# Optimization experiments

Hardware: AMD Instinct MI355X
Metric: run time of the kernel (lower is better)

Reference implementation:

```python
import jax, jax.numpy as jnp
import numpy as np

TEXT_VOCAB = 32000
CB = 1024          # audio_codebook_size
NCB = 8            # audio_num_codebooks
H = 2048           # hidden_size
NH = 16            # attention heads
NKV = 4            # kv heads (GQA)
HD = H // NH       # head dim = 128
FF = 8192          # ffn intermediate
L = 2              # num layers
EPS = 1e-5


def rmsnorm(x, w):
    v = jnp.mean(x * x, axis=-1, keepdims=True)
    return x * jax.lax.rsqrt(v + EPS) * w


def rope(x, pos):
    # x: [B,S,h,d], rotate-half style RoPE
    d = x.shape[-1]
    inv = 1.0 / (10000.0 ** (jnp.arange(0, d, 2, dtype=jnp.float32) / d))
    ang = pos[:, None] * inv[None, :]                 # [S, d/2]
    cos = jnp.cos(ang)[None, :, None, :]
    sin = jnp.sin(ang)[None, :, None, :]
    x1, x2 = x[..., : d // 2], x[..., d // 2 :]
    return jnp.concatenate([x1 * cos - x2 * sin, x2 * cos + x1 * sin], axis=-1)


def attention(x, wq, wk, wv, wo, pos, mask_bias):
    B, S, _ = x.shape
    q = (x @ wq).reshape(B, S, NH, HD)
    k = (x @ wk).reshape(B, S, NKV, HD)
    v = (x @ wv).reshape(B, S, NKV, HD)
    q = rope(q, pos)
    k = rope(k, pos)
    k = jnp.repeat(k, NH // NKV, axis=2)
    v = jnp.repeat(v, NH // NKV, axis=2)
    scores = jnp.einsum('bqhd,bkhd->bhqk', q, k) / np.float32(np.sqrt(HD))
    p = jax.nn.softmax(scores + mask_bias, axis=-1)
    o = jnp.einsum('bhqk,bkhd->bqhd', p, v).reshape(B, S, NH * HD)
    return o @ wo


def mlp(x, wfc, wproj):
    return jax.nn.silu(x @ wfc) @ wproj


def setup_inputs() -> dict:
    key = jax.random.key(0)
    ks = jax.random.split(key, 20)
    s = 0.02
    inp = {
        'input_ids': jax.random.randint(ks[0], (1, 2048), 0, TEXT_VOCAB + CB, dtype=jnp.int64 if jax.config.jax_enable_x64 else jnp.int32),
        'vocab_emb': jax.random.normal(ks[1], (TEXT_VOCAB, H), jnp.float32) * s,
        'audio_emb': jax.random.normal(ks[2], (NCB * CB, H), jnp.float32) * s,
        'ln_in_text': jnp.ones((L, H), jnp.float32),
        'ln_in_audio': jnp.ones((L, H), jnp.float32),
        'ln_post_text': jnp.ones((L, H), jnp.float32),
        'ln_post_audio': jnp.ones((L, H), jnp.float32),
        'wq': jax.random.normal(ks[3], (L, H, NH * HD), jnp.float32) * s,
        'wk': jax.random.normal(ks[4], (L, H, NKV * HD), jnp.float32) * s,
        'wv': jax.random.normal(ks[5], (L, H, NKV * HD), jnp.float32) * s,
        'wo': jax.random.normal(ks[6], (L, NH * HD, H), jnp.float32) * s,
        'wfc_text': jax.random.normal(ks[7], (L, H, FF), jnp.float32) * s,
        'wproj_text': jax.random.normal(ks[8], (L, FF, H), jnp.float32) * s,
        'wfc_audio': jax.random.normal(ks[9], (L, H, FF), jnp.float32) * s,
        'wproj_audio': jax.random.normal(ks[10], (L, FF, H), jnp.float32) * s,
        'ln_f': jnp.ones((H,), jnp.float32),
    }
    return inp


def reference(input_ids, vocab_emb, audio_emb, ln_in_text, ln_in_audio,
              ln_post_text, ln_post_audio, wq, wk, wv, wo,
              wfc_text, wproj_text, wfc_audio, wproj_audio, ln_f):
    B, S = input_ids.shape
    amask = input_ids > TEXT_VOCAB - 1                      # [B,S] audio-token mask
    text_tok = jnp.where(amask, TEXT_VOCAB - 1, input_ids)
    text_e = vocab_emb[text_tok]                            # [B,S,H]
    audio_tok = jnp.where(amask, input_ids - TEXT_VOCAB, 0)
    shift = (jnp.arange(NCB) * CB)[:, None, None]           # [NCB,1,1]
    audio_e = audio_emb[audio_tok[None] + shift].sum(0)     # sum over codebooks -> [B,S,H]
    h = jnp.where(amask[..., None], audio_e, text_e)

    pos = jnp.arange(S, dtype=jnp.float32)
    causal = jnp.tril(jnp.ones((S, S), bool))
    mask_bias = jnp.where(causal, 0.0, -1e9).astype(jnp.float32)[None, None]
    m = amask[..., None]

    for i in range(L):
        res = h
        hn = jnp.where(m, rmsnorm(h, ln_in_audio[i]), rmsnorm(h, ln_in_text[i]))
        h = res + attention(hn, wq[i], wk[i], wv[i], wo[i], pos, mask_bias)
        res = h
        t = mlp(rmsnorm(h, ln_post_text[i]), wfc_text[i], wproj_text[i])
        a = mlp(rmsnorm(h, ln_post_audio[i]), wfc_audio[i], wproj_audio[i])
        h = res + jnp.where(m, a, t)

    return rmsnorm(h, ln_f)
```

## Files before the change

kernel.cpp:

```cpp
#include <hip/hip_runtime.h>
#include <hip/hip_bf16.h>
#include <math.h>

#define S_LEN 2048
#define HID   2048

typedef __bf16 bf16x8 __attribute__((ext_vector_type(8)));
typedef float  f32x4  __attribute__((ext_vector_type(4)));

__device__ __forceinline__ unsigned short f2b(float x) {
  __hip_bfloat16 h = __float2bfloat16(x);
  return __builtin_bit_cast(unsigned short, h);
}

__device__ __forceinline__ float block_sum_256(float v) {
  __shared__ float red[4];
  #pragma unroll
  for (int o = 32; o > 0; o >>= 1) v += __shfl_down(v, o, 64);
  if ((threadIdx.x & 63) == 0) red[threadIdx.x >> 6] = v;
  __syncthreads();
  v = red[0] + red[1] + red[2] + red[3];
  __syncthreads();
  return v;
}

__global__ __launch_bounds__(256) void embed_kernel(
    const int* __restrict__ ids, const float* __restrict__ vemb,
    const float* __restrict__ aemb, float* __restrict__ h, int* __restrict__ amask) {
  const int s = blockIdx.x;
  const int id = ids[s];
  const bool am = id > 31999;
  if (threadIdx.x == 0) amask[s] = am ? 1 : 0;
  const int d0 = threadIdx.x * 8;
  float out[8];
  if (am) {
    const int at = id - 32000;
    #pragma unroll
    for (int u = 0; u < 8; u++) out[u] = 0.f;
    for (int cb = 0; cb < 8; cb++) {
      const float* src = aemb + (long)(at + cb * 1024) * HID + d0;
      #pragma unroll
      for (int u = 0; u < 8; u++) out[u] += src[u];
    }
  } else {
    const float* src = vemb + (long)id * HID + d0;
    #pragma unroll
    for (int u = 0; u < 8; u++) out[u] = src[u];
  }
  float* dst = h + (long)s * HID + d0;
  #pragma unroll
  for (int u = 0; u < 8; u++) dst[u] = out[u];
}

__global__ __launch_bounds__(256) void partition_rows(
    const int* __restrict__ ids, int* __restrict__ apos, int* __restrict__ cnt) {
  __shared__ int ca[256];
  __shared__ int sc[257];
  const int t = threadIdx.x;
  int m[8], loc = 0;
  #pragma unroll
  for (int i = 0; i < 8; i++) { m[i] = ids[t * 8 + i] > 31999 ? 1 : 0; loc += m[i]; }
  ca[t] = loc;
  __syncthreads();
  if (t == 0) {
    int run = 0;
    for (int i = 0; i < 256; i++) { sc[i] = run; run += ca[i]; }
    sc[256] = run;
  }
  __syncthreads();
  int off = sc[t];
  #pragma unroll
  for (int i = 0; i < 8; i++) {
    const int s = t * 8 + i;
    if (m[i]) { apos[s] = off; off++; }
    else apos[s] = -1;
  }
  if (t == 0) { cnt[0] = sc[256]; cnt[1] = (sc[256] + 127) & ~127; }
}

__global__ void init_ctrs(int* c) { c[threadIdx.x] = 0; }

__global__ __launch_bounds__(256) void transposew(
    const float* __restrict__ W, int ldw, unsigned short* __restrict__ Wt, int K, int N) {
  __shared__ float t[64][65];
  const int k0 = blockIdx.y * 64, n0 = blockIdx.x * 64;
  const int q = threadIdx.x & 15;
  const int r0 = threadIdx.x >> 4;
  #pragma unroll
  for (int i = 0; i < 4; i++) {
    const int row = r0 + i * 16;
    const float4 v = *(const float4*)(W + (long)(k0 + row) * ldw + n0 + q * 4);
    t[row][q * 4 + 0] = v.x; t[row][q * 4 + 1] = v.y;
    t[row][q * 4 + 2] = v.z; t[row][q * 4 + 3] = v.w;
  }
  __syncthreads();
  #pragma unroll
  for (int i = 0; i < 4; i++) {
    const int n = r0 + i * 16;
    ushort4 o;
    o.x = f2b(t[q * 4 + 0][n]); o.y = f2b(t[q * 4 + 1][n]);
    o.z = f2b(t[q * 4 + 2][n]); o.w = f2b(t[q * 4 + 3][n]);
    *(ushort4*)(Wt + (long)(n0 + n) * K + k0 + q * 4) = o;
  }
}

__global__ __launch_bounds__(256) void rope_table(float* __restrict__ c, float* __restrict__ s_) {
  const int i = blockIdx.x * 256 + threadIdx.x;
  const int pos = i >> 6, j = i & 63;
  const float inv = powf(10000.f, -(float)(2 * j) * (1.f / 128.f));
  const float ang = (float)pos * inv;
  c[i] = cosf(ang);
  s_[i] = sinf(ang);
}

__global__ __launch_bounds__(64) void rope_apply(
    const float* __restrict__ qkv, const float* __restrict__ rc, const float* __restrict__ rs,
    unsigned short* __restrict__ qb, unsigned short* __restrict__ kb) {
  const int s = blockIdx.x;
  const int hh = blockIdx.y;
  const int j = threadIdx.x;
  const float c = rc[s * 64 + j], sn = rs[s * 64 + j];
  const float* base;
  unsigned short* out;
  if (hh < 16) {
    base = qkv + (long)s * 3072 + hh * 128;
    out = qb + (long)s * 2048 + hh * 128;
  } else {
    base = qkv + (long)s * 3072 + 2048 + (hh - 16) * 128;
    out = kb + (long)s * 512 + (hh - 16) * 128;
  }
  const float x1 = base[j], x2 = base[j + 64];
  out[j] = f2b(x1 * c - x2 * sn);
  out[j + 64] = f2b(x2 * c + x1 * sn);
}

__global__ __launch_bounds__(256) void rmsnorm_sel(
    const float* __restrict__ x, const int* __restrict__ amask,
    const float* __restrict__ wt, const float* __restrict__ wa, unsigned short* __restrict__ out) {
  const long s = blockIdx.x;
  const float* xr = x + s * HID;
  const int d0 = threadIdx.x * 8;
  float v[8], ss = 0.f;
  #pragma unroll
  for (int u = 0; u < 8; u++) { v[u] = xr[d0 + u]; ss += v[u] * v[u]; }
  ss = block_sum_256(ss) * (1.f / HID);
  const float rr = rsqrtf(ss + 1e-5f);
  const float* w = amask[s] ? wa : wt;
  #pragma unroll
  for (int u = 0; u < 8; u++) out[s * HID + d0 + u] = f2b(v[u] * rr * w[d0 + u]);
}

__global__ __launch_bounds__(256) void rmsnorm_post(
    const float* __restrict__ x, const int* __restrict__ apos,
    const float* __restrict__ wt, const float* __restrict__ wa,
    unsigned short* __restrict__ hnt, unsigned short* __restrict__ hna_g) {
  const long s = blockIdx.x;
  const float* xr = x + s * HID;
  const int d0 = threadIdx.x * 8;
  float v[8], ss = 0.f;
  #pragma unroll
  for (int u = 0; u < 8; u++) { v[u] = xr[d0 + u]; ss += v[u] * v[u]; }
  ss = block_sum_256(ss) * (1.f / HID);
  const float rr = rsqrtf(ss + 1e-5f);
  const int ap = apos[s];
  #pragma unroll
  for (int u = 0; u < 8; u++) {
    const float xn = v[u] * rr;
    hnt[s * HID + d0 + u] = f2b(xn * wt[d0 + u]);
    if (ap >= 0) hna_g[(long)ap * HID + d0 + u] = f2b(xn * wa[d0 + u]);
  }
}

__global__ __launch_bounds__(256) void rmsnorm_final(
    const float* __restrict__ x, const float* __restrict__ w, float* __restrict__ out) {
  const long s = blockIdx.x;
  const float* xr = x + s * HID;
  const int d0 = threadIdx.x * 8;
  float v[8], ss = 0.f;
  #pragma unroll
  for (int u = 0; u < 8; u++) { v[u] = xr[d0 + u]; ss += v[u] * v[u]; }
  ss = block_sum_256(ss) * (1.f / HID);
  const float rr = rsqrtf(ss + 1e-5f);
  #pragma unroll
  for (int u = 0; u < 8; u++) out[s * HID + d0 + u] = v[u] * rr * w[d0 + u];
}

__device__ __forceinline__ void gload16(const void* g, void* l) {
  __builtin_amdgcn_global_load_lds((const __attribute__((address_space(1))) void*)g,
                                   (__attribute__((address_space(3))) void*)l, 16, 0, 0);
}

#define ABAR() do { __builtin_amdgcn_s_barrier(); \
  asm volatile("" ::: "memory"); __builtin_amdgcn_sched_barrier(0); } while (0)

__global__ __launch_bounds__(256) void attn_pass1(
    const unsigned short* __restrict__ qb, const unsigned short* __restrict__ kb,
    float* __restrict__ mstat, int* __restrict__ ctr, float iscale) {
  __shared__ __align__(16) unsigned short Kb[2][2][128][64];
  __shared__ int s_item;
  const int tid = threadIdx.x;
  const int lane = tid & 63;
  const int w = tid >> 6;
  const int lr = lane & 15;
  const int kg = lane >> 4;
  const int trow = tid >> 3;
  const int tc = tid & 7;

  for (;;) {
    if (tid == 0) s_item = atomicAdd(ctr, 1);
    __syncthreads();
    const int item = s_item;
    __syncthreads();
    if (item >= 512) break;
    const int q64 = 31 - (item >> 4);
    const int h = item & 15;
    const int kvh = h >> 2;
    const int bm = q64 * 64;
    const int nt = (bm >> 7) + 1;

    bf16x8 af_q[4];
    {
      const unsigned short* qr = qb + (long)(bm + w * 16 + lr) * 2048 + h * 128 + kg * 8;
      #pragma unroll
      for (int c = 0; c < 4; c++) af_q[c] = *(const bf16x8*)(qr + c * 32);
    }
    float m[4], l[4];
    #pragma unroll
    for (int r = 0; r < 4; r++) { m[r] = -1e30f; l[r] = 0.f; }

    auto stageK = [&](int buf, int t) {
      const int kv0 = t * 128;
      #pragma unroll
      for (int hh2 = 0; hh2 < 2; hh2++)
        #pragma unroll
        for (int rr = 0; rr < 4; rr++) {
          const int row = trow + rr * 32;
          gload16(kb + (long)(kv0 + row) * 512 + kvh * 128 + hh2 * 64 + ((tc ^ (row & 7)) * 8),
                  &Kb[buf][hh2][row][tc * 8]);
        }
    };

    stageK(0, 0);
    for (int t = 0; t < nt; t++) {
      const bool hn = (t + 1) < nt;
      if (hn) stageK((t + 1) & 1, t + 1);
      if (hn) { asm volatile("s_waitcnt vmcnt(8)" ::: "memory"); }
      else    { asm volatile("s_waitcnt vmcnt(0)" ::: "memory"); }
      ABAR();
      f32x4 acc[8];
      #pragma unroll
      for (int nf = 0; nf < 8; nf++) acc[nf] = (f32x4){0.f, 0.f, 0.f, 0.f};
      #pragma unroll
      for (int c = 0; c < 4; c++) {
        #pragma unroll
        for (int nf = 0; nf < 8; nf++) {
          const int row = nf * 16 + lr;
          bf16x8 bk = *(const bf16x8*)(&Kb[t & 1][c >> 1][row][(((c & 1) * 4 + kg) ^ (row & 7)) * 8]);
          acc[nf] = __builtin_amdgcn_mfma_f32_16x16x32_bf16(af_q[c], bk, acc[nf], 0, 0, 0);
        }
      }
      const bool diag = !hn;
      #pragma unroll
      for (int r = 0; r < 4; r++) {
        const int rowg = bm + w * 16 + kg * 4 + r;
        float sv[8], tmax = -1e30f;
        #pragma unroll
        for (int nf = 0; nf < 8; nf++) {
          float s = acc[nf][r] * iscale;
          const int colg = t * 128 + nf * 16 + lr;
          if (diag && colg > rowg) s = -1e30f;
          sv[nf] = s;
          tmax = fmaxf(tmax, s);
        }
        #pragma unroll
        for (int o = 1; o < 16; o <<= 1) tmax = fmaxf(tmax, __shfl_xor(tmax, o, 64));
        const float mn = fmaxf(m[r], tmax);
        float psum = 0.f;
        #pragma unroll
        for (int nf = 0; nf < 8; nf++) psum += __expf(sv[nf] - mn);
        #pragma unroll
        for (int o = 1; o < 16; o <<= 1) psum += __shfl_xor(psum, o, 64);
        l[r] = l[r] * __expf(m[r] - mn) + psum;
        m[r] = mn;
      }
      ABAR();
    }
    if (lr == 0) {
      #pragma unroll
      for (int r = 0; r < 4; r++)
        mstat[h * 2048 + bm + w * 16 + kg * 4 + r] = m[r] + __logf(l[r]);
    }
    __syncthreads();
  }
}

__global__ __launch_bounds__(512, 1) void attn_pass2(
    const unsigned short* __restrict__ qb, const unsigned short* __restrict__ kb,
    const unsigned short* __restrict__ vt, const float* __restrict__ mstat,
    float* __restrict__ opart, int* __restrict__ ctr, float iscale) {
  __shared__ __align__(16) unsigned short Kb[2][2][128][64];
  __shared__ __align__(16) unsigned short Vb[2][128][64];
  __shared__ __align__(16) unsigned short Pb[8][16][144];
  __shared__ int s_item;
  const int tid = threadIdx.x;
  const int lane = tid & 63;
  const int w = tid >> 6;
  const int lr = lane & 15;
  const int kg = lane >> 4;
  const int trow = tid >> 3;
  const int tc = tid & 7;

  for (;;) {
    if (tid == 0) s_item = atomicAdd(ctr, 1);
    __syncthreads();
    const int item = s_item;
    __syncthreads();
    if (item >= 512) break;
    const int qq = 15 - (item >> 5);
    const int h = item & 15;
    const int cch = (item >> 4) & 1;
    const int kvh = h >> 2;
    const int bm = qq * 128;
    const int nt = qq + 1;
    const int tmid = (nt + 1) >> 1;
    const int t0 = cch ? tmid : 0;
    const int t1 = cch ? nt : tmid;
    if (t0 >= t1) continue;

    bf16x8 af_q[4];
    {
      const unsigned short* qr = qb + (long)(bm + w * 16 + lr) * 2048 + h * 128 + kg * 8;
      #pragma unroll
      for (int c = 0; c < 4; c++) af_q[c] = *(const bf16x8*)(qr + c * 32);
    }
    float mm_r[4];
    #pragma unroll
    for (int r = 0; r < 4; r++) mm_r[r] = mstat[h * 2048 + bm + w * 16 + kg * 4 + r];
    f32x4 acc_o[8];
    #pragma unroll
    for (int nf = 0; nf < 8; nf++) acc_o[nf] = (f32x4){0.f, 0.f, 0.f, 0.f};

    auto stageK = [&](int buf, int t) {
      const int kv0 = t * 128;
      #pragma unroll
      for (int hh2 = 0; hh2 < 2; hh2++)
        #pragma unroll
        for (int rr = 0; rr < 2; rr++) {
          const int row = trow + rr * 64;
          gload16(kb + (long)(kv0 + row) * 512 + kvh * 128 + hh2 * 64 + ((tc ^ (row & 7)) * 8),
                  &Kb[buf][hh2][row][tc * 8]);
        }
    };
    auto stageV = [&](int t) {
      const int kv0 = t * 128;
      #pragma unroll
      for (int hh2 = 0; hh2 < 2; hh2++)
        #pragma unroll
        for (int rr = 0; rr < 2; rr++) {
          const int row = trow + rr * 64;
          gload16(vt + (long)(kvh * 128 + row) * 2048 + kv0 + hh2 * 64 + ((tc ^ (row & 7)) * 8),
                  &Vb[hh2][row][tc * 8]);
        }
    };

    stageK(t0 & 1, t0);
    for (int t = t0; t < t1; t++) {
      const bool hn = (t + 1) < t1;
      stageV(t);
      if (hn) stageK((t + 1) & 1, t + 1);
      if (hn) { asm volatile("s_waitcnt vmcnt(8)" ::: "memory"); }
      else    { asm volatile("s_waitcnt vmcnt(4)" ::: "memory"); }
      ABAR();
      f32x4 acc[8];
      #pragma unroll
      for (int nf = 0; nf < 8; nf++) acc[nf] = (f32x4){0.f, 0.f, 0.f, 0.f};
      #pragma unroll
      for (int c = 0; c < 4; c++) {
        #pragma unroll
        for (int nf = 0; nf < 8; nf++) {
          const int row = nf * 16 + lr;
          bf16x8 bk = *(const bf16x8*)(&Kb[t & 1][c >> 1][row][(((c & 1) * 4 + kg) ^ (row & 7)) * 8]);
          acc[nf] = __builtin_amdgcn_mfma_f32_16x16x32_bf16(af_q[c], bk, acc[nf], 0, 0, 0);
        }
      }
      const bool diag = (t == nt - 1);
      #pragma unroll
      for (int nf = 0; nf < 8; nf++) {
        #pragma unroll
        for (int r = 0; r < 4; r++) {
          float s = acc[nf][r] * iscale;
          const int colg = t * 128 + nf * 16 + lr;
          const int rowg = bm + w * 16 + kg * 4 + r;
          if (diag && colg > rowg) s = -1e30f;
          Pb[w][kg * 4 + r][nf * 16 + lr] = f2b(__expf(s - mm_r[r]));
        }
      }
      asm volatile("s_waitcnt lgkmcnt(0)" ::: "memory");
      __builtin_amdgcn_sched_barrier(0);
      if (hn) { asm volatile("s_waitcnt vmcnt(4)" ::: "memory"); }
      else    { asm volatile("s_waitcnt vmcnt(0)" ::: "memory"); }
      ABAR();
      #pragma unroll
      for (int c = 0; c < 4; c++) {
        bf16x8 ap = *(const bf16x8*)(&Pb[w][lr][c * 32 + kg * 8]);
        #pragma unroll
        for (int nf = 0; nf < 8; nf++) {
          const int row = nf * 16 + lr;
          bf16x8 bv = *(const bf16x8*)(&Vb[c >> 1][row][(((c & 1) * 4 + kg) ^ (row & 7)) * 8]);
          acc_o[nf] = __builtin_amdgcn_mfma_f32_16x16x32_bf16(ap, bv, acc_o[nf], 0, 0, 0);
        }
      }
      ABAR();
    }
    float* op = opart + (long)cch * 4194304;
    #pragma unroll
    for (int nf = 0; nf < 8; nf++)
      #pragma unroll
      for (int r = 0; r < 4; r++)
        op[(long)(bm + w * 16 + kg * 4 + r) * 2048 + h * 128 + nf * 16 + lr] = acc_o[nf][r];
    __syncthreads();
  }
}

__global__ __launch_bounds__(256) void o_merge(
    const float* __restrict__ op, unsigned short* __restrict__ o) {
  const int i = blockIdx.x * 256 + threadIdx.x;
  const int row = i >> 11;
  float v = op[i];
  if (row >= 128) v += op[4194304 + i];
  o[i] = f2b(v);
}

__global__ __launch_bounds__(256) void mlp_reduce(
    const float* __restrict__ pt, const float* __restrict__ pa,
    const int* __restrict__ apos, float* __restrict__ h) {
  const int i = blockIdx.x * 256 + threadIdx.x;
  const int r = i >> 11, c = i & 2047;
  const long Z = (long)1 << 22;
  const int ap = apos[r];
  float val;
  if (ap < 0) {
    val = pt[i] + pt[i + Z] + pt[i + 2 * Z] + pt[i + 3 * Z];
  } else {
    const long b = (long)ap * 2048 + c;
    val = 0.f;
    #pragma unroll
    for (int k = 0; k < 8; k++) val += pa[k * Z + b];
  }
  h[i] += val;
}

template <int BM, int BN, int EPI>
__global__ __launch_bounds__(512) void gemm2(
    const unsigned short* __restrict__ A, int lda, long sAz,
    const unsigned short* __restrict__ Bt, int ldb, long sBz,
    void* __restrict__ Cv, int ldc, long sCz, long sCx, int K, float scale,
    const int* __restrict__ ecnt, int kspl) {
  constexpr int MF = BM / 32;
  constexpr int NF = BN / 64;
  __shared__ __align__(16) unsigned short smem[2 * (BM + BN) * 64];
  const int tid = threadIdx.x;
  const int lane = tid & 63;
  const int wave = tid >> 6;
  const int bm = blockIdx.y * BM;
  const int z = blockIdx.z;
  int bn, kbeg, nt;
  if constexpr (EPI == 7) {
    bn = blockIdx.x * BN;
    kbeg = z * kspl;
    nt = kspl / 64;
  } else {
    bn = blockIdx.x * BN;
    kbeg = 0;
    nt = K / 64;
  }
  if constexpr (EPI == 2 || EPI == 7) {
    if (bm >= ecnt[1]) return;
  }
  A += sAz * z;
  Bt += sBz * z;
  const int wm = (wave >> 2) * (BM / 2);
  const int wn = (wave & 3) * (BN / 4);
  const int lr = lane & 15;
  const int kg = lane >> 4;
  const int swx = lr & 7;
  const int trow = tid >> 3;
  const int tc = tid & 7;
  const long aoff = (long)(bm + trow) * lda + ((tc ^ (trow & 7)) * 8);
  const long boff = (long)(bn + trow) * ldb + ((tc ^ (trow & 7)) * 8);

  f32x4 acc[MF][NF];
  #pragma unroll
  for (int m = 0; m < MF; m++)
    #pragma unroll
    for (int n = 0; n < NF; n++) acc[m][n] = (f32x4){0.f, 0.f, 0.f, 0.f};

  auto stage = [&](int buf, int k0) {
    unsigned short* sA = &smem[(size_t)buf * (BM + BN) * 64];
    #pragma unroll
    for (int r = 0; r < BM / 64; r++)
      gload16(A + aoff + (long)r * 64 * lda + k0, sA + r * 4096 + tid * 8);
    unsigned short* sB = sA + BM * 64;
    #pragma unroll
    for (int r = 0; r < BN / 64; r++)
      gload16(Bt + boff + (long)r * 64 * ldb + k0, sB + r * 4096 + tid * 8);
  };
  auto compute = [&](int buf) {
    const unsigned short* sA = &smem[(size_t)buf * (BM + BN) * 64];
    const unsigned short* sB = sA + BM * 64;
    #pragma unroll
    for (int ks = 0; ks < 2; ks++) {
      bf16x8 af[MF], bv[NF];
      #pragma unroll
      for (int m = 0; m < MF; m++) {
        const int row = wm + m * 16 + lr;
        af[m] = *(const bf16x8*)(sA + row * 64 + (((ks * 4 + kg) ^ swx) * 8));
      }
      #pragma unroll
      for (int n = 0; n < NF; n++) {
        const int row = wn + n * 16 + lr;
        bv[n] = *(const bf16x8*)(sB + row * 64 + (((ks * 4 + kg) ^ swx) * 8));
      }
      #pragma unroll
      for (int m = 0; m < MF; m++)
        #pragma unroll
        for (int n = 0; n < NF; n++)
          acc[m][n] = __builtin_amdgcn_mfma_f32_16x16x32_bf16(af[m], bv[n], acc[m][n], 0, 0, 0);
    }
  };

  if (nt > 0) {
    stage(0, kbeg);
    asm volatile("s_waitcnt vmcnt(0)" ::: "memory");
    __syncthreads();
    int cur = 0;
    for (int t = 0; t < nt; t++) {
      if (t + 1 < nt) stage(cur ^ 1, kbeg + (t + 1) * 64);
      compute(cur);
      asm volatile("s_waitcnt vmcnt(0)" ::: "memory");
      __syncthreads();
      cur ^= 1;
    }
  }

  #pragma unroll
  for (int m = 0; m < MF; m++) {
    #pragma unroll
    for (int n = 0; n < NF; n++) {
      #pragma unroll
      for (int r = 0; r < 4; r++) {
        const int grow = bm + wm + m * 16 + kg * 4 + r;
        const int gcol = bn + wn + n * 16 + lr;
        const long idx = (long)grow * ldc + gcol;
        float v = acc[m][n][r];
        if constexpr (EPI == 0) {
          ((float*)Cv)[sCz * z + idx] = v;
        } else if constexpr (EPI == 2) {
          ((unsigned short*)Cv)[idx] = f2b(v / (1.f + expf(-v)));
        } else if constexpr (EPI == 3) {
          ((float*)Cv)[idx] += v;
        } else if constexpr (EPI == 7) {
          ((float*)Cv)[(long)z * sCz + idx] = v;
        }
      }
    }
  }
}

template <int EPI>
__global__ __launch_bounds__(512, 1) void gemm8(
    const unsigned short* __restrict__ A0, const unsigned short* __restrict__ A1, int lda,
    const unsigned short* __restrict__ Bt, long sBz, int ldb,
    void* __restrict__ Cv, int ldc, long sCz, int K) {
  __shared__ __align__(16) unsigned short smem[2][4][8192];
  const int tid = threadIdx.x;
  const int lane = tid & 63;
  const int wave = tid >> 6;
  const int bm = blockIdx.y * 256;
  const int bn = blockIdx.x * 256;
  const int z = blockIdx.z;
  const unsigned short* Aq;
  const unsigned short* Bq;
  if constexpr (EPI == 10) {
    Aq = z ? A1 : A0;
    Bq = Bt + (long)z * sBz;
  } else {
    Aq = A0 + z * 2048;
    Bq = Bt + z * 2048;
  }
  const int nt = K / 64;
  const int trow = tid >> 3;
  const int tc = tid & 7;
  const int sws = (tc ^ (trow & 7)) * 8;
  const int lr = lane & 15;
  const int kg = lane >> 4;
  const int wr = (wave >> 2) * 64;
  const int wc = (wave & 3) * 32;

  f32x4 acc[2][2][4][2];
  #pragma unroll
  for (int mh = 0; mh < 2; mh++)
    #pragma unroll
    for (int nh = 0; nh < 2; nh++)
      #pragma unroll
      for (int mf = 0; mf < 4; mf++)
        #pragma unroll
        for (int nf = 0; nf < 2; nf++) acc[mh][nh][mf][nf] = (f32x4){0.f, 0.f, 0.f, 0.f};

  bf16x8 af[2][4], bv0[2][2], bv1[2][2];

  auto stageA = [&](int buf, int half, int k0) {
    const unsigned short* g = Aq + (long)(bm + half * 128 + trow) * lda + k0 + sws;
    unsigned short* l = &smem[buf][half][0] + tid * 8;
    gload16(g, l);
    gload16(g + (long)64 * lda, l + 4096);
  };
  auto stageB = [&](int buf, int half, int k0) {
    const unsigned short* g = Bq + (long)(bn + half * 128 + trow) * ldb + k0 + sws;
    unsigned short* l = &smem[buf][2 + half][0] + tid * 8;
    gload16(g, l);
    gload16(g + (long)64 * ldb, l + 4096);
  };

#define GSYNC(VM) \
  asm volatile("s_waitcnt vmcnt(" #VM ")" ::: "memory"); \
  __builtin_amdgcn_s_barrier(); \
  asm volatile("" ::: "memory"); \
  __builtin_amdgcn_sched_barrier(0)

#define RD_A(BUF, MH) do { \
    _Pragma("unroll") \
    for (int ks = 0; ks < 2; ++ks) { \
      _Pragma("unroll") \
      for (int mf = 0; mf < 4; ++mf) { \
        const int row = wr + mf * 16 + lr; \
        af[ks][mf] = *(const bf16x8*)(&smem[BUF][MH][0] + row * 64 + (((ks * 4 + kg) ^ (row & 7)) * 8)); \
      } \
    } \
  } while (0)

#define RD_B(BUF, NH, BV) do { \
    _Pragma("unroll") \
    for (int ks = 0; ks < 2; ++ks) { \
      _Pragma("unroll") \
      for (int nf = 0; nf < 2; ++nf) { \
        const int row = wc + nf * 16 + lr; \
        BV[ks][nf] = *(const bf16x8*)(&smem[BUF][2 + NH][0] + row * 64 + (((ks * 4 + kg) ^ (row & 7)) * 8)); \
      } \
    } \
  } while (0)

#define DO_MFMA(MH, NH, BV) do { \
    __builtin_amdgcn_s_setprio(1); \
    _Pragma("unroll") \
    for (int ks = 0; ks < 2; ++ks) \
      _Pragma("unroll") \
      for (int mf = 0; mf < 4; ++mf) \
        _Pragma("unroll") \
        for (int nf = 0; nf < 2; ++nf) \
          acc[MH][NH][mf][nf] = __builtin_amdgcn_mfma_f32_16x16x32_bf16( \
              af[ks][mf], BV[ks][nf], acc[MH][NH][mf][nf], 0, 0, 0); \
    __builtin_amdgcn_s_setprio(0); \
  } while (0)

  stageA(0, 0, 0); stageB(0, 0, 0); stageB(0, 1, 0); stageA(0, 1, 0);
  stageA(1, 0, 64); stageB(1, 0, 64); stageB(1, 1, 64);
  GSYNC(10);

  for (int t = 0; t <= nt - 3; ++t) {
    const int b = t & 1, nb = b ^ 1;
    const int k1 = (t + 1) << 6, k2 = (t + 2) << 6;
    RD_A(b, 0); RD_B(b, 0, bv0); stageA(nb, 1, k1); DO_MFMA(0, 0, bv0); GSYNC(10);
    RD_B(b, 1, bv1);             stageA(b, 0, k2);  DO_MFMA(0, 1, bv1); GSYNC(10);
    RD_A(b, 1);                  stageB(b, 0, k2);  DO_MFMA(1, 1, bv1); GSYNC(10);
                                 stageB(b, 1, k2);  DO_MFMA(1, 0, bv0); GSYNC(10);
  }
  {
    const int t = nt - 2;
    const int b = t & 1, nb = b ^ 1;
    const int k1 = (t + 1) << 6;
    RD_A(b, 0); RD_B(b, 0, bv0); stageA(nb, 1, k1); DO_MFMA(0, 0, bv0); GSYNC(10);
    RD_B(b, 1, bv1);                                DO_MFMA(0, 1, bv1); GSYNC(8);
    RD_A(b, 1);                                     DO_MFMA(1, 1, bv1); GSYNC(8);
                                                    DO_MFMA(1, 0, bv0); GSYNC(4);
  }
  {
    const int b = (nt - 1) & 1;
    RD_A(b, 0); RD_B(b, 0, bv0); DO_MFMA(0, 0, bv0); GSYNC(2);
    RD_B(b, 1, bv1);             DO_MFMA(0, 1, bv1); GSYNC(0);
    RD_A(b, 1);                  DO_MFMA(1, 1, bv1); GSYNC(0);
                                 DO_MFMA(1, 0, bv0);
  }
#undef DO_MFMA
#undef RD_B
#undef RD_A
#undef GSYNC

  #pragma unroll
  for (int mh = 0; mh < 2; mh++) {
    #pragma unroll
    for (int nh = 0; nh < 2; nh++) {
      #pragma unroll
      for (int mf = 0; mf < 4; mf++) {
        #pragma unroll
        for (int nf = 0; nf < 2; nf++) {
          #pragma unroll
          for (int r = 0; r < 4; r++) {
            const int grow = bm + mh * 128 + wr + mf * 16 + kg * 4 + r;
            const int gcol = bn + nh * 128 + wc + nf * 16 + lr;
            const long idx = (long)z * sCz + (long)grow * ldc + gcol;
            const float v = acc[mh][nh][mf][nf][r];
            if constexpr (EPI == 10) {
              ((unsigned short*)Cv)[idx] = f2b(v / (1.f + expf(-v)));
            } else {
              ((float*)Cv)[idx] = v;
            }
          }
        }
      }
    }
  }
}

__global__ __launch_bounds__(256) void fill_zero(float* p, long n) {
  const long i = (long)blockIdx.x * 256 + threadIdx.x;
  if (i < n) p[i] = 0.f;
}

extern "C" void kernel_launch(void* const* d_in, const int* in_sizes, int n_in,
                              void* d_out, int out_size, void* d_ws, size_t ws_size,
                              hipStream_t stream) {
  const int* ids = (const int*)d_in[0];
  const float* vocab_emb = (const float*)d_in[1];
  const float* audio_emb = (const float*)d_in[2];
  const float* ln_in_text = (const float*)d_in[3];
  const float* ln_in_audio = (const float*)d_in[4];
  const float* ln_post_text = (const float*)d_in[5];
  const float* ln_post_audio = (const float*)d_in[6];
  const float* wq = (const float*)d_in[7];
  const float* wk = (const float*)d_in[8];
  const float* wv = (const float*)d_in[9];
  const float* wo = (const float*)d_in[10];
  const float* wfc_t = (const float*)d_in[11];
  const float* wpj_t = (const float*)d_in[12];
  const float* wfc_a = (const float*)d_in[13];
  const float* wpj_a = (const float*)d_in[14];
  const float* ln_f = (const float*)d_in[15];

  size_t off = 0;
  auto alloc = [&](size_t bytes) -> void* {
    void* p = (char*)d_ws + off;
    off += (bytes + 255) & ~(size_t)255;
    return p;
  };
  const size_t LW = 77594624;
  unsigned short* wsT = (unsigned short*)alloc((size_t)2 * LW * 2);
  int* amask = (int*)alloc(S_LEN * 4);
  int* apos = (int*)alloc(S_LEN * 4);
  int* cnt = (int*)alloc(16);
  int* ctrs = (int*)alloc(16);
  float* ropec = (float*)alloc((size_t)S_LEN * 64 * 4);
  float* ropes = (float*)alloc((size_t)S_LEN * 64 * 4);
  float* h = (float*)alloc((size_t)S_LEN * HID * 4);
  unsigned short* hn = (unsigned short*)alloc((size_t)S_LEN * HID * 2);
  unsigned short* hnt = (unsigned short*)alloc((size_t)S_LEN * HID * 2);
  unsigned short* hna_g = (unsigned short*)alloc((size_t)S_LEN * HID * 2);
  float* qkv = (float*)alloc((size_t)S_LEN * 3072 * 4);
  unsigned short* qb = (unsigned short*)alloc((size_t)S_LEN * 2048 * 2);
  unsigned short* kb = (unsigned short*)alloc((size_t)S_LEN * 512 * 2);
  unsigned short* vt = (unsigned short*)alloc((size_t)512 * S_LEN * 2);
  unsigned short* o = (unsigned short*)alloc((size_t)S_LEN * 2048 * 2);
  float* mstat = (float*)alloc((size_t)16 * 2048 * 4);
  char* big = (char*)alloc(268435456);
  float* opart = (float*)big;
  unsigned short* mlp_t = (unsigned short*)big;
  unsigned short* mlp_a = (unsigned short*)(big + 33554432);
  float* pt = (float*)(big + 67108864);
  float* pa = (float*)(big + 134217728);

  if (ws_size < off) {
    fill_zero<<<(out_size + 255) / 256, 256, 0, stream>>>((float*)d_out, out_size);
    return;
  }

  const size_t WO_ = 6291456, WFT = 10485760, WPT = 27262976, WFA = 44040192, WPA = 60817408;

  embed_kernel<<<S_LEN, 256, 0, stream>>>(ids, vocab_emb, audio_emb, h, amask);
  partition_rows<<<1, 256, 0, stream>>>(ids, apos, cnt);
  init_ctrs<<<1, 4, 0, stream>>>(ctrs);
  rope_table<<<S_LEN * 64 / 256, 256, 0, stream>>>(ropec, ropes);

  for (int i = 0; i < 2; i++) {
    const size_t wb = (size_t)i * LW;
    transposew<<<dim3(32, 32), 256, 0, stream>>>(wq + (size_t)i * 2048 * 2048, 2048, wsT + wb, 2048, 2048);
    transposew<<<dim3(8, 32), 256, 0, stream>>>(wk + (size_t)i * 2048 * 512, 512, wsT + wb + 4194304, 2048, 512);
    transposew<<<dim3(8, 32), 256, 0, stream>>>(wv + (size_t)i * 2048 * 512, 512, wsT + wb + 5242880, 2048, 512);
    transposew<<<dim3(32, 32), 256, 0, stream>>>(wo + (size_t)i * 2048 * 2048, 2048, wsT + wb + WO_, 2048, 2048);
    transposew<<<dim3(128, 32), 256, 0, stream>>>(wfc_t + (size_t)i * 2048 * 8192, 8192, wsT + wb + WFT, 2048, 8192);
    transposew<<<dim3(32, 128), 256, 0, stream>>>(wpj_t + (size_t)i * 8192 * 2048, 2048, wsT + wb + WPT, 8192, 2048);
    transposew<<<dim3(128, 32), 256, 0, stream>>>(wfc_a + (size_t)i * 2048 * 8192, 8192, wsT + wb + WFA, 2048, 8192);
    transposew<<<dim3(32, 128), 256, 0, stream>>>(wpj_a + (size_t)i * 8192 * 2048, 2048, wsT + wb + WPA, 8192, 2048);
  }

  const float iscale = 0.08838834764831845f;
  for (int i = 0; i < 2; i++) {
    const size_t wb = (size_t)i * LW;
    rmsnorm_sel<<<S_LEN, 256, 0, stream>>>(h, amask, ln_in_text + i * HID, ln_in_audio + i * HID, hn);
    gemm2<128, 128, 0><<<dim3(24, 16, 1), 512, 0, stream>>>(hn, 2048, 0, wsT + wb, 2048, 0,
        qkv, 3072, 0, 0, 2048, 1.f, nullptr, 0);
    rope_apply<<<dim3(S_LEN, 20), 64, 0, stream>>>(qkv, ropec, ropes, qb, kb);
    transposew<<<dim3(8, 32), 256, 0, stream>>>(qkv + 2560, 3072, vt, 2048, 512);
    attn_pass1<<<256, 256, 0, stream>>>(qb, kb, mstat, ctrs + i * 2, iscale);
    attn_pass2<<<256, 512, 0, stream>>>(qb, kb, vt, mstat, opart, ctrs + i * 2 + 1, iscale);
    o_merge<<<16384, 256, 0, stream>>>(opart, o);
    gemm2<128, 128, 3><<<dim3(16, 16, 1), 512, 0, stream>>>(o, 2048, 0, wsT + wb + WO_, 2048, 0,
        h, 2048, 0, 0, 2048, 1.f, nullptr, 0);
    rmsnorm_post<<<S_LEN, 256, 0, stream>>>(h, apos, ln_post_text + i * HID, ln_post_audio + i * HID, hnt, hna_g);
    gemm2<128, 128, 2><<<dim3(64, 16, 1), 512, 0, stream>>>(hna_g, 2048, 0, wsT + wb + WFA, 2048, 0,
        mlp_a, 8192, 0, 0, 2048, 1.f, cnt, 0);
    gemm8<10><<<dim3(32, 8, 1), 512, 0, stream>>>(hnt, hnt, 2048, wsT + wb + WFT, 0, 2048,
        mlp_t, 8192, 0, 2048);
    gemm2<128, 128, 7><<<dim3(16, 16, 8), 512, 0, stream>>>(mlp_a, 8192, 0, wsT + wb + WPA, 8192, 0,
        pa, 2048, (long)1 << 22, 0, 8192, 1.f, cnt, 1024);
    gemm8<11><<<dim3(8, 8, 4), 512, 0, stream>>>(mlp_t, mlp_t, 8192, wsT + wb + WPT, 0, 8192,
        pt, 2048, (long)1 << 22, 2048);
    mlp_reduce<<<16384, 256, 0, stream>>>(pt, pa, apos, h);
  }
  rmsnorm_final<<<S_LEN, 256, 0, stream>>>(h, ln_f, (float*)d_out);
}
```

Before: 1.070 ms.

## Fuse RoPE into QKV GEMM epilogue and switch attention to single-pass online softmax

The QKV GEMM now applies RoPE in its epilogue and writes bf16 Q/K/V directly, which removes the fp32 qkv buffer and the separate rope_apply kernel. V is transposed by a small bf16 transpose. The two-pass attention (a stats pass followed by an output pass) becomes one flash-style online-softmax kernel. It writes per-chunk m and l, and the merge kernel rescales and normalizes the two split partials. This cuts one full QK^T recomputation and some memory traffic, at the cost of extra rescaling work in the inner loop and a stats buffer that needs initialization.

```diff
diff --git a/kernel.cpp b/kernel.cpp
--- a/kernel.cpp
+++ b/kernel.cpp
@@ -80,6 +80,12 @@
 
 __global__ void init_ctrs(int* c) { c[threadIdx.x] = 0; }
 
+__global__ __launch_bounds__(256) void init_stats(float* __restrict__ stm, float* __restrict__ stl) {
+  const int i = blockIdx.x * 256 + threadIdx.x;
+  stm[i] = -1e30f;
+  stl[i] = 0.f;
+}
+
 __global__ __launch_bounds__(256) void transposew(
     const float* __restrict__ W, int ldw, unsigned short* __restrict__ Wt, int K, int N) {
   __shared__ float t[64][65];
@@ -101,6 +107,30 @@
     o.x = f2b(t[q * 4 + 0][n]); o.y = f2b(t[q * 4 + 1][n]);
     o.z = f2b(t[q * 4 + 2][n]); o.w = f2b(t[q * 4 + 3][n]);
     *(ushort4*)(Wt + (long)(n0 + n) * K + k0 + q * 4) = o;
+  }
+}
+
+__global__ __launch_bounds__(256) void transpose_b16(
+    const unsigned short* __restrict__ V, unsigned short* __restrict__ Vt) {
+  __shared__ unsigned short t[64][72];
+  const int s0 = blockIdx.y * 64, d0 = blockIdx.x * 64;
+  const int q = threadIdx.x & 15;
+  const int r0 = threadIdx.x >> 4;
+  #pragma unroll
+  for (int i = 0; i < 4; i++) {
+    const int row = r0 + i * 16;
+    const ushort4 v = *(const ushort4*)(V + (long)(s0 + row) * 512 + d0 + q * 4);
+    t[row][q * 4 + 0] = v.x; t[row][q * 4 + 1] = v.y;
+    t[row][q * 4 + 2] = v.z; t[row][q * 4 + 3] = v.w;
+  }
+  __syncthreads();
+  #pragma unroll
+  for (int i = 0; i < 4; i++) {
+    const int d = r0 + i * 16;
+    ushort4 o;
+    o.x = t[q * 4 + 0][d]; o.y = t[q * 4 + 1][d];
+    o.z = t[q * 4 + 2][d]; o.w = t[q * 4 + 3][d];
+    *(ushort4*)(Vt + (long)(d0 + d) * 2048 + s0 + q * 4) = o;
   }
 }
 
@@ -111,27 +141,6 @@
   const float ang = (float)pos * inv;
   c[i] = cosf(ang);
   s_[i] = sinf(ang);
-}
-
-__global__ __launch_bounds__(64) void rope_apply(
-    const float* __restrict__ qkv, const float* __restrict__ rc, const float* __restrict__ rs,
-    unsigned short* __restrict__ qb, unsigned short* __restrict__ kb) {
-  const int s = blockIdx.x;
-  const int hh = blockIdx.y;
-  const int j = threadIdx.x;
-  const float c = rc[s * 64 + j], sn = rs[s * 64 + j];
-  const float* base;
-  unsigned short* out;
-  if (hh < 16) {
-    base = qkv + (long)s * 3072 + hh * 128;
-    out = qb + (long)s * 2048 + hh * 128;
-  } else {
-    base = qkv + (long)s * 3072 + 2048 + (hh - 16) * 128;
-    out = kb + (long)s * 512 + (hh - 16) * 128;
-  }
-  const float x1 = base[j], x2 = base[j + 64];
-  out[j] = f2b(x1 * c - x2 * sn);
-  out[j + 64] = f2b(x2 * c + x1 * sn);
 }
 
 __global__ __launch_bounds__(256) void rmsnorm_sel(
@@ -193,111 +202,11 @@
 #define ABAR() do { __builtin_amdgcn_s_barrier(); \
   asm volatile("" ::: "memory"); __builtin_amdgcn_sched_barrier(0); } while (0)
 
-__global__ __launch_bounds__(256) void attn_pass1(
+__global__ __launch_bounds__(512, 1) void attn_flash(
     const unsigned short* __restrict__ qb, const unsigned short* __restrict__ kb,
-    float* __restrict__ mstat, int* __restrict__ ctr, float iscale) {
-  __shared__ __align__(16) unsigned short Kb[2][2][128][64];
-  __shared__ int s_item;
-  const int tid = threadIdx.x;
-  const int lane = tid & 63;
-  const int w = tid >> 6;
-  const int lr = lane & 15;
-  const int kg = lane >> 4;
-  const int trow = tid >> 3;
-  const int tc = tid & 7;
-
-  for (;;) {
-    if (tid == 0) s_item = atomicAdd(ctr, 1);
-    __syncthreads();
-    const int item = s_item;
-    __syncthreads();
-    if (item >= 512) break;
-    const int q64 = 31 - (item >> 4);
-    const int h = item & 15;
-    const int kvh = h >> 2;
-    const int bm = q64 * 64;
-    const int nt = (bm >> 7) + 1;
-
-    bf16x8 af_q[4];
-    {
-      const unsigned short* qr = qb + (long)(bm + w * 16 + lr) * 2048 + h * 128 + kg * 8;
-      #pragma unroll
-      for (int c = 0; c < 4; c++) af_q[c] = *(const bf16x8*)(qr + c * 32);
-    }
-    float m[4], l[4];
-    #pragma unroll
-    for (int r = 0; r < 4; r++) { m[r] = -1e30f; l[r] = 0.f; }
-
-    auto stageK = [&](int buf, int t) {
-      const int kv0 = t * 128;
-      #pragma unroll
-      for (int hh2 = 0; hh2 < 2; hh2++)
-        #pragma unroll
-        for (int rr = 0; rr < 4; rr++) {
-          const int row = trow + rr * 32;
-          gload16(kb + (long)(kv0 + row) * 512 + kvh * 128 + hh2 * 64 + ((tc ^ (row & 7)) * 8),
-                  &Kb[buf][hh2][row][tc * 8]);
-        }
-    };
-
-    stageK(0, 0);
-    for (int t = 0; t < nt; t++) {
-      const bool hn = (t + 1) < nt;
-      if (hn) stageK((t + 1) & 1, t + 1);
-      if (hn) { asm volatile("s_waitcnt vmcnt(8)" ::: "memory"); }
-      else    { asm volatile("s_waitcnt vmcnt(0)" ::: "memory"); }
-      ABAR();
-      f32x4 acc[8];
-      #pragma unroll
-      for (int nf = 0; nf < 8; nf++) acc[nf] = (f32x4){0.f, 0.f, 0.f, 0.f};
-      #pragma unroll
-      for (int c = 0; c < 4; c++) {
-        #pragma unroll
-        for (int nf = 0; nf < 8; nf++) {
-          const int row = nf * 16 + lr;
-          bf16x8 bk = *(const bf16x8*)(&Kb[t & 1][c >> 1][row][(((c & 1) * 4 + kg) ^ (row & 7)) * 8]);
-          acc[nf] = __builtin_amdgcn_mfma_f32_16x16x32_bf16(af_q[c], bk, acc[nf], 0, 0, 0);
-        }
-      }
-      const bool diag = !hn;
-      #pragma unroll
-      for (int r = 0; r < 4; r++) {
-        const int rowg = bm + w * 16 + kg * 4 + r;
-        float sv[8], tmax = -1e30f;
-        #pragma unroll
-        for (int nf = 0; nf < 8; nf++) {
-          float s = acc[nf][r] * iscale;
-          const int colg = t * 128 + nf * 16 + lr;
-          if (diag && colg > rowg) s = -1e30f;
-          sv[nf] = s;
-          tmax = fmaxf(tmax, s);
-        }
-        #pragma unroll
-        for (int o = 1; o < 16; o <<= 1) tmax = fmaxf(tmax, __shfl_xor(tmax, o, 64));
-        const float mn = fmaxf(m[r], tmax);
-        float psum = 0.f;
-        #pragma unroll
-        for (int nf = 0; nf < 8; nf++) psum += __expf(sv[nf] - mn);
-        #pragma unroll
-        for (int o = 1; o < 16; o <<= 1) psum += __shfl_xor(psum, o, 64);
-        l[r] = l[r] * __expf(m[r] - mn) + psum;
-        m[r] = mn;
-      }
-      ABAR();
-    }
-    if (lr == 0) {
-      #pragma unroll
-      for (int r = 0; r < 4; r++)
-        mstat[h * 2048 + bm + w * 16 + kg * 4 + r] = m[r] + __logf(l[r]);
-    }
-    __syncthreads();
-  }
-}
-
-__global__ __launch_bounds__(512, 1) void attn_pass2(
-    const unsigned short* __restrict__ qb, const unsigned short* __restrict__ kb,
-    const unsigned short* __restrict__ vt, const float* __restrict__ mstat,
-    float* __restrict__ opart, int* __restrict__ ctr, float iscale) {
+    const unsigned short* __restrict__ vt, float* __restrict__ opart,
+    float* __restrict__ stm, float* __restrict__ stl,
+    int* __restrict__ ctr, float iscale) {
   __shared__ __align__(16) unsigned short Kb[2][2][128][64];
   __shared__ __align__(16) unsigned short Vb[2][128][64];
   __shared__ __align__(16) unsigned short Pb[8][16][144];
@@ -333,9 +242,9 @@
       #pragma unroll
       for (int c = 0; c < 4; c++) af_q[c] = *(const bf16x8*)(qr + c * 32);
     }
-    float mm_r[4];
-    #pragma unroll
-    for (int r = 0; r < 4; r++) mm_r[r] = mstat[h * 2048 + bm + w * 16 + kg * 4 + r];
+    float m[4], l[4];
+    #pragma unroll
+    for (int r = 0; r < 4; r++) { m[r] = -1e30f; l[r] = 0.f; }
     f32x4 acc_o[8];
     #pragma unroll
     for (int nf = 0; nf < 8; nf++) acc_o[nf] = (f32x4){0.f, 0.f, 0.f, 0.f};
@@ -385,15 +294,34 @@
       }
       const bool diag = (t == nt - 1);
       #pragma unroll
-      for (int nf = 0; nf < 8; nf++) {
-        #pragma unroll
-        for (int r = 0; r < 4; r++) {
+      for (int r = 0; r < 4; r++) {
+        const int rowg = bm + w * 16 + kg * 4 + r;
+        float sv[8], tmax = -1e30f;
+        #pragma unroll
+        for (int nf = 0; nf < 8; nf++) {
           float s = acc[nf][r] * iscale;
           const int colg = t * 128 + nf * 16 + lr;
-          const int rowg = bm + w * 16 + kg * 4 + r;
           if (diag && colg > rowg) s = -1e30f;
-          Pb[w][kg * 4 + r][nf * 16 + lr] = f2b(__expf(s - mm_r[r]));
+          sv[nf] = s;
+          tmax = fmaxf(tmax, s);
         }
+        #pragma unroll
+        for (int o = 1; o < 16; o <<= 1) tmax = fmaxf(tmax, __shfl_xor(tmax, o, 64));
+        const float mn = fmaxf(m[r], tmax);
+        const float scal = __expf(m[r] - mn);
+        float psum = 0.f;
+        #pragma unroll
+        for (int nf = 0; nf < 8; nf++) {
+          const float pe = __expf(sv[nf] - mn);
+          psum += pe;
+          Pb[w][kg * 4 + r][nf * 16 + lr] = f2b(pe);
+        }
+        #pragma unroll
+        for (int o = 1; o < 16; o <<= 1) psum += __shfl_xor(psum, o, 64);
+        l[r] = l[r] * scal + psum;
+        m[r] = mn;
+        #pragma unroll
+        for (int nf = 0; nf < 8; nf++) acc_o[nf][r] *= scal;
       }
       asm volatile("s_waitcnt lgkmcnt(0)" ::: "memory");
       __builtin_amdgcn_sched_barrier(0);
@@ -418,17 +346,30 @@
       #pragma unroll
       for (int r = 0; r < 4; r++)
         op[(long)(bm + w * 16 + kg * 4 + r) * 2048 + h * 128 + nf * 16 + lr] = acc_o[nf][r];
+    if (lr == 0) {
+      #pragma unroll
+      for (int r = 0; r < 4; r++) {
+        const int row = bm + w * 16 + kg * 4 + r;
+        stm[(cch * 16 + h) * 2048 + row] = m[r];
+        stl[(cch * 16 + h) * 2048 + row] = l[r];
+      }
+    }
     __syncthreads();
   }
 }
 
-__global__ __launch_bounds__(256) void o_merge(
-    const float* __restrict__ op, unsigned short* __restrict__ o) {
+__global__ __launch_bounds__(256) void o_merge2(
+    const float* __restrict__ op, const float* __restrict__ stm,
+    const float* __restrict__ stl, unsigned short* __restrict__ o) {
   const int i = blockIdx.x * 256 + threadIdx.x;
-  const int row = i >> 11;
-  float v = op[i];
-  if (row >= 128) v += op[4194304 + i];
-  o[i] = f2b(v);
+  const int s = i >> 11, c = i & 2047, h = c >> 7;
+  const int si = h * 2048 + s;
+  const float m1 = stm[si], l1 = stl[si];
+  const float m2 = stm[32768 + si], l2 = stl[32768 + si];
+  const float M = fmaxf(m1, m2);
+  const float w1 = __expf(m1 - M), w2 = __expf(m2 - M);
+  const float denom = l1 * w1 + l2 * w2;
+  o[i] = f2b((op[i] * w1 + op[i + 4194304] * w2) / denom);
 }
 
 __global__ __launch_bounds__(256) void mlp_reduce(
@@ -455,7 +396,9 @@
     const unsigned short* __restrict__ A, int lda, long sAz,
     const unsigned short* __restrict__ Bt, int ldb, long sBz,
     void* __restrict__ Cv, int ldc, long sCz, long sCx, int K, float scale,
-    const int* __restrict__ ecnt, int kspl) {
+    const int* __restrict__ ecnt, int kspl,
+    const float* __restrict__ rc, const float* __restrict__ rs,
+    unsigned short* __restrict__ kbo, unsigned short* __restrict__ vbo) {
   constexpr int MF = BM / 32;
   constexpr int NF = BN / 64;
   __shared__ __align__(16) unsigned short smem[2 * (BM + BN) * 64];
@@ -543,6 +486,50 @@
     }
   }
 
+  if constexpr (EPI == 8) {
+    if (bn >= 2560) {
+      #pragma unroll
+      for (int m = 0; m < MF; m++)
+        #pragma unroll
+        for (int n = 0; n < NF; n++)
+          #pragma unroll
+          for (int r = 0; r < 4; r++) {
+            const int grow = bm + wm + m * 16 + kg * 4 + r;
+            const int gcol = bn + wn + n * 16 + lr;
+            vbo[(long)grow * 512 + (gcol - 2560)] = f2b(acc[m][n][r]);
+          }
+    } else {
+      float* Cl = (float*)smem;
+      #pragma unroll
+      for (int m = 0; m < MF; m++)
+        #pragma unroll
+        for (int n = 0; n < NF; n++)
+          #pragma unroll
+          for (int r = 0; r < 4; r++)
+            Cl[(wm + m * 16 + kg * 4 + r) * 128 + wn + n * 16 + lr] = acc[m][n][r];
+      __syncthreads();
+      const int j = tid & 63;
+      const int r2 = tid >> 6;
+      #pragma unroll
+      for (int it = 0; it < 16; it++) {
+        const int row = r2 + it * 8;
+        const int s = bm + row;
+        const float c = rc[s * 64 + j], sn = rs[s * 64 + j];
+        const float x1 = Cl[row * 128 + j], x2 = Cl[row * 128 + j + 64];
+        const unsigned short o1 = f2b(x1 * c - x2 * sn);
+        const unsigned short o2 = f2b(x2 * c + x1 * sn);
+        if (bn < 2048) {
+          unsigned short* qp = (unsigned short*)Cv + (long)s * 2048 + bn + j;
+          qp[0] = o1; qp[64] = o2;
+        } else {
+          unsigned short* kp = kbo + (long)s * 512 + (bn - 2048) + j;
+          kp[0] = o1; kp[64] = o2;
+        }
+      }
+    }
+    return;
+  }
+
   #pragma unroll
   for (int m = 0; m < MF; m++) {
     #pragma unroll
@@ -553,9 +540,7 @@
         const int gcol = bn + wn + n * 16 + lr;
         const long idx = (long)grow * ldc + gcol;
         float v = acc[m][n][r];
-        if constexpr (EPI == 0) {
-          ((float*)Cv)[sCz * z + idx] = v;
-        } else if constexpr (EPI == 2) {
+        if constexpr (EPI == 2) {
           ((unsigned short*)Cv)[idx] = f2b(v / (1.f + expf(-v)));
         } else if constexpr (EPI == 3) {
           ((float*)Cv)[idx] += v;
@@ -765,12 +750,13 @@
   unsigned short* hn = (unsigned short*)alloc((size_t)S_LEN * HID * 2);
   unsigned short* hnt = (unsigned short*)alloc((size_t)S_LEN * HID * 2);
   unsigned short* hna_g = (unsigned short*)alloc((size_t)S_LEN * HID * 2);
-  float* qkv = (float*)alloc((size_t)S_LEN * 3072 * 4);
   unsigned short* qb = (unsigned short*)alloc((size_t)S_LEN * 2048 * 2);
   unsigned short* kb = (unsigned short*)alloc((size_t)S_LEN * 512 * 2);
+  unsigned short* vb = (unsigned short*)alloc((size_t)S_LEN * 512 * 2);
   unsigned short* vt = (unsigned short*)alloc((size_t)512 * S_LEN * 2);
   unsigned short* o = (unsigned short*)alloc((size_t)S_LEN * 2048 * 2);
-  float* mstat = (float*)alloc((size_t)16 * 2048 * 4);
+  float* stm = (float*)alloc((size_t)2 * 16 * 2048 * 4);
+  float* stl = (float*)alloc((size_t)2 * 16 * 2048 * 4);
   char* big = (char*)alloc(268435456);
   float* opart = (float*)big;
   unsigned short* mlp_t = (unsigned short*)big;
@@ -788,6 +774,7 @@
   embed_kernel<<<S_LEN, 256, 0, stream>>>(ids, vocab_emb, audio_emb, h, amask);
   partition_rows<<<1, 256, 0, stream>>>(ids, apos, cnt);
   init_ctrs<<<1, 4, 0, stream>>>(ctrs);
+  init_stats<<<256, 256, 0, stream>>>(stm, stl);
   rope_table<<<S_LEN * 64 / 256, 256, 0, stream>>>(ropec, ropes);
 
   for (int i = 0; i < 2; i++) {
@@ -806,22 +793,20 @@
   for (int i = 0; i < 2; i++) {
     const size_t wb = (size_t)i * LW;
     rmsnorm_sel<<<S_LEN, 256, 0, stream>>>(h, amask, ln_in_text + i * HID, ln_in_audio + i * HID, hn);
-    gemm2<128, 128, 0><<<dim3(24, 16, 1), 512, 0, stream>>>(hn, 2048, 0, wsT + wb, 2048, 0,
-        qkv, 3072, 0, 0, 2048, 1.f, nullptr, 0);
-    rope_apply<<<dim3(S_LEN, 20), 64, 0, stream>>>(qkv, ropec, ropes, qb, kb);
-    transposew<<<dim3(8, 32), 256, 0, stream>>>(qkv + 2560, 3072, vt, 2048, 512);
-    attn_pass1<<<256, 256, 0, stream>>>(qb, kb, mstat, ctrs + i * 2, iscale);
-    attn_pass2<<<256, 512, 0, stream>>>(qb, kb, vt, mstat, opart, ctrs + i * 2 + 1, iscale);
-    o_merge<<<16384, 256, 0, stream>>>(opart, o);
+    gemm2<128, 128, 8><<<dim3(24, 16, 1), 512, 0, stream>>>(hn, 2048, 0, wsT + wb, 2048, 0,
+        qb, 2048, 0, 0, 2048, 1.f, nullptr, 0, ropec, ropes, kb, vb);
+    transpose_b16<<<dim3(8, 32), 256, 0, stream>>>(vb, vt);
+    attn_flash<<<256, 512, 0, stream>>>(qb, kb, vt, opart, stm, stl, ctrs + i, iscale);
+    o_merge2<<<16384, 256, 0, stream>>>(opart, stm, stl, o);
     gemm2<128, 128, 3><<<dim3(16, 16, 1), 512, 0, stream>>>(o, 2048, 0, wsT + wb + WO_, 2048, 0,
-        h, 2048, 0, 0, 2048, 1.f, nullptr, 0);
+        h, 2048, 0, 0, 2048, 1.f, nullptr, 0, nullptr, nullptr, nullptr, nullptr);
     rmsnorm_post<<<S_LEN, 256, 0, stream>>>(h, apos, ln_post_text + i * HID, ln_post_audio + i * HID, hnt, hna_g);
     gemm2<128, 128, 2><<<dim3(64, 16, 1), 512, 0, stream>>>(hna_g, 2048, 0, wsT + wb + WFA, 2048, 0,
-        mlp_a, 8192, 0, 0, 2048, 1.f, cnt, 0);
+        mlp_a, 8192, 0, 0, 2048, 1.f, cnt, 0, nullptr, nullptr, nullptr, nullptr);
     gemm8<10><<<dim3(32, 8, 1), 512, 0, stream>>>(hnt, hnt, 2048, wsT + wb + WFT, 0, 2048,
         mlp_t, 8192, 0, 2048);
     gemm2<128, 128, 7><<<dim3(16, 16, 8), 512, 0, stream>>>(mlp_a, 8192, 0, wsT + wb + WPA, 8192, 0,
-        pa, 2048, (long)1 << 22, 0, 8192, 1.f, cnt, 1024);
+        pa, 2048, (long)1 << 22, 0, 8192, 1.f, cnt, 1024, nullptr, nullptr, nullptr, nullptr);
     gemm8<11><<<dim3(8, 8, 4), 512, 0, stream>>>(mlp_t, mlp_t, 8192, wsT + wb + WPT, 0, 8192,
         pt, 2048, (long)1 << 22, 2048);
     mlp_reduce<<<16384, 256, 0, stream>>>(pt, pa, apos, h);
```

Measured after the change: 986.4 us. -7.8%, faster.
